# Performance work log

Measured on AMD Instinct MI355X. Metric: run time of the kernel, lower is better.

Reference implementation:

```python
import jax, jax.numpy as jnp
import numpy as np

B, S, D, H = 2, 4096, 512, 8
DH = D // H
EPS = 1e-5


def setup_inputs() -> dict:
    key = jax.random.key(0)
    ks = jax.random.split(key, 8)
    s = 0.02
    return {
        "x": jax.random.normal(ks[0], (B, S, D), jnp.float32),
        "in_proj_w": jax.random.normal(ks[1], (3 * D, D), jnp.float32) * s,
        "in_proj_b": jnp.zeros((3 * D,), jnp.float32),
        "out_proj_w": jax.random.normal(ks[2], (D, D), jnp.float32) * s,
        "out_proj_b": jnp.zeros((D,), jnp.float32),
        "ln1_g": jnp.ones((D,), jnp.float32),
        "ln1_b": jnp.zeros((D,), jnp.float32),
        "ln2_g": jnp.ones((D,), jnp.float32),
        "ln2_b": jnp.zeros((D,), jnp.float32),
        "w1": jax.random.normal(ks[3], (D, D), jnp.float32) * s,
        "b1": jnp.zeros((D,), jnp.float32),
        "w2": jax.random.normal(ks[4], (D, D), jnp.float32) * s,
        "b2": jnp.zeros((D,), jnp.float32),
        "window": 256,
    }


def _layernorm(x, g, b):
    mu = jnp.mean(x, axis=-1, keepdims=True)
    var = jnp.mean(jnp.square(x - mu), axis=-1, keepdims=True)
    return (x - mu) * jax.lax.rsqrt(var + EPS) * g + b


def reference(x, in_proj_w, in_proj_b, out_proj_w, out_proj_b,
              ln1_g, ln1_b, ln2_g, ln2_b, w1, b1, w2, b2, window):
    b, s, d = x.shape
    # sliding-window mask: allowed iff |i - j| <= window
    idx = jnp.arange(s)
    allowed = jnp.abs(idx[:, None] - idx[None, :]) <= window  # [S,S]

    # fused QKV projection (torch MultiheadAttention layout: W [3D, D])
    qkv = x @ in_proj_w.T + in_proj_b  # [B,S,3D]
    q, k, v = jnp.split(qkv, 3, axis=-1)
    q = q.reshape(b, s, H, DH)
    k = k.reshape(b, s, H, DH)
    v = v.reshape(b, s, H, DH)

    scale = 1.0 / jnp.sqrt(jnp.float32(DH))
    scores = jnp.einsum("bqhd,bkhd->bhqk", q, k) * scale  # [B,H,S,S]
    scores = jnp.where(allowed[None, None], scores, -jnp.inf)
    attn = jax.nn.softmax(scores, axis=-1)
    ctx = jnp.einsum("bhqk,bkhd->bqhd", attn, v).reshape(b, s, d)
    attn_out = ctx @ out_proj_w.T + out_proj_b

    # residual + LayerNorm (dropout rate 0 -> identity)
    h = _layernorm(x + attn_out, ln1_g, ln1_b)
    mlp = jax.nn.relu(h @ w1.T + b1) @ w2.T + b2
    return _layernorm(h + mlp, ln2_g, ln2_b)
```

## Files before the change

### kernel.cpp

```cpp
#include <hip/hip_runtime.h>

typedef __bf16 bf16;
typedef __bf16 bf16x2 __attribute__((ext_vector_type(2)));
typedef __bf16 bf16x8 __attribute__((ext_vector_type(8)));
typedef float f32x4 __attribute__((ext_vector_type(4)));

#define S_LEN 4096
#define DMODEL 512
#define NHEAD 8
#define DHEAD 64
#define BATCH 2
#define M_ROWS (BATCH * S_LEN)
#define K_DIM 512
#define QKV_LD 1536

__device__ __forceinline__ void async16(void* lds, const void* g) {
  __builtin_amdgcn_global_load_lds(
      (const __attribute__((address_space(1))) unsigned int*)g,
      (__attribute__((address_space(3))) unsigned int*)lds, 16, 0, 0);
}

__global__ void detect_dtype(const unsigned int* __restrict__ x,
                             int* __restrict__ flag) {
  const int lane = threadIdx.x;
  int cnt = 0;
#pragma unroll
  for (int i = 0; i < 16; ++i) {
    const unsigned int w = x[lane * 16 + i];
    const unsigned int e = (w >> 7) & 0xFFu;
    cnt += (e >= 100u && e <= 140u) ? 1 : 0;
  }
#pragma unroll
  for (int off = 1; off < 64; off <<= 1) cnt += __shfl_xor(cnt, off);
  if (lane == 0) *flag = (cnt >= 700) ? 1 : 0;
}

__device__ __forceinline__ bf16x8 ld8(const void* p, size_t e, bool asF32) {
  if (asF32) {
    const float* q = (const float*)p + e;
    const float4 a = *(const float4*)q;
    const float4 b = *(const float4*)(q + 4);
    bf16x8 r;
    r[0] = (bf16)a.x; r[1] = (bf16)a.y; r[2] = (bf16)a.z; r[3] = (bf16)a.w;
    r[4] = (bf16)b.x; r[5] = (bf16)b.y; r[6] = (bf16)b.z; r[7] = (bf16)b.w;
    return r;
  }
  return *(const bf16x8*)((const bf16*)p + e);
}

__device__ __forceinline__ float ld1(const void* p, size_t e, bool asF32) {
  return asF32 ? ((const float*)p)[e] : (float)((const bf16*)p)[e];
}

__global__ __launch_bounds__(256) void cvt_weights(const void* __restrict__ s0,
                                                   const void* __restrict__ s1,
                                                   const void* __restrict__ s2,
                                                   const void* __restrict__ s3,
                                                   bf16* __restrict__ dst,
                                                   const int* __restrict__ flag) {
  const bool f32in = (*flag == 0);
  const int b = blockIdx.x;
  const void* s;
  size_t doff;
  int lb;
  if (b < 384)      { s = s0; doff = 0;        lb = b; }
  else if (b < 512) { s = s1; doff = 786432;   lb = b - 384; }
  else if (b < 640) { s = s2; doff = 1048576;  lb = b - 512; }
  else              { s = s3; doff = 1310720;  lb = b - 640; }
  const size_t idx = (size_t)lb * 2048 + threadIdx.x * 8;
  *(bf16x8*)(dst + doff + idx) = ld8(s, idx, f32in);
}

__global__ __launch_bounds__(256) void cvt_x(const void* __restrict__ x,
                                             bf16* __restrict__ xb,
                                             const int* __restrict__ flag) {
  const bool f32in = (*flag == 0);
  const size_t idx = ((size_t)blockIdx.x * 256 + threadIdx.x) * 8;
  *(bf16x8*)(xb + idx) = ld8(x, idx, f32in);
}

template <int BN, bool RELU>
__global__ __launch_bounds__(256) void gemm_bt(const bf16* __restrict__ A,
                                               const bf16* __restrict__ W,
                                               const void* __restrict__ bias,
                                               bf16* __restrict__ C, int N,
                                               const int* __restrict__ flag) {
  __shared__ __align__(16) bf16 As[128 * 64];
  __shared__ __align__(16) bf16 Ws[BN * 64];

  const bool f32in = (*flag == 0);

  const int t = threadIdx.x;
  const int lane = t & 63;
  const int wave = t >> 6;
  constexpr int MT = (BN == 128) ? 4 : 2;
  const int wm = (BN == 128) ? (wave >> 1) * 64 : wave * 32;
  const int wn = (BN == 128) ? (wave & 1) * 64 : 0;
  const int l16 = lane & 15;
  const int quad = lane >> 4;
  const int m0 = blockIdx.y * 128;
  const int n0 = blockIdx.x * BN;

  const int rr = lane >> 3;
  const int cb = (lane & 7) ^ rr;
  const int sw = l16 & 7;

  f32x4 acc[MT][4];
#pragma unroll
  for (int i = 0; i < MT; ++i)
#pragma unroll
    for (int j = 0; j < 4; ++j) acc[i][j] = (f32x4){0.f, 0.f, 0.f, 0.f};

  for (int kt = 0; kt < K_DIM; kt += 64) {
    __syncthreads();
#pragma unroll
    for (int i = 0; i < 4; ++i) {
      const int r0 = wave * 32 + i * 8;
      async16(&As[r0 * 64], &A[(size_t)(m0 + r0 + rr) * K_DIM + kt + cb * 8]);
    }
#pragma unroll
    for (int i = 0; i < BN / 32; ++i) {
      const int r0 = wave * (BN / 4) + i * 8;
      async16(&Ws[r0 * 64], &W[(size_t)(n0 + r0 + rr) * K_DIM + kt + cb * 8]);
    }
    __syncthreads();
#pragma unroll
    for (int ks = 0; ks < 2; ++ks) {
      bf16x8 af[MT], wf[4];
#pragma unroll
      for (int mt = 0; mt < MT; ++mt)
        af[mt] = *(const bf16x8*)&As[(wm + mt * 16 + l16) * 64 +
                                     (((ks * 4 + quad) ^ sw) * 8)];
#pragma unroll
      for (int nt = 0; nt < 4; ++nt)
        wf[nt] = *(const bf16x8*)&Ws[(wn + nt * 16 + l16) * 64 +
                                     (((ks * 4 + quad) ^ sw) * 8)];
#pragma unroll
      for (int mt = 0; mt < MT; ++mt)
#pragma unroll
        for (int nt = 0; nt < 4; ++nt)
          acc[mt][nt] = __builtin_amdgcn_mfma_f32_16x16x32_bf16(af[mt], wf[nt],
                                                                acc[mt][nt], 0, 0, 0);
    }
  }

#pragma unroll
  for (int nt = 0; nt < 4; ++nt) {
    const int n = n0 + wn + nt * 16 + l16;
    const float bv = ld1(bias, n, f32in);
#pragma unroll
    for (int mt = 0; mt < MT; ++mt) {
#pragma unroll
      for (int r = 0; r < 4; ++r) {
        const int m = m0 + wm + mt * 16 + quad * 4 + r;
        float v = acc[mt][nt][r] + bv;
        if (RELU) v = fmaxf(v, 0.f);
        C[(size_t)m * N + n] = (bf16)v;
      }
    }
  }
}

__global__ __launch_bounds__(256) void attn_fwd(const bf16* __restrict__ qkv,
                                                bf16* __restrict__ ctx,
                                                const int* __restrict__ wptr) {
  __shared__ __align__(16) bf16 Vt[2][64][72];
  __shared__ __align__(16) bf16 Pbuf[4][16][72];

  const int t = threadIdx.x;
  const int lane = t & 63;
  const int wave = t >> 6;
  const int l16 = lane & 15;
  const int quad = lane >> 4;

  const int nqb = S_LEN / 64;
  const int qblk = blockIdx.x % nqb;
  const int h = (blockIdx.x / nqb) % NHEAD;
  const int b = blockIdx.x / (nqb * NHEAD);
  const int qbase = qblk * 64;
  int window = *wptr;
  if (window < 0) window = 0;
  if (window > S_LEN) window = S_LEN;
  const float scale = 0.125f;

  const int qrow = qbase + wave * 16 + l16;
  const bf16* qp = qkv + (size_t)(b * S_LEN + qrow) * QKV_LD + h * DHEAD;
  const bf16x8 qf0 = *(const bf16x8*)(qp + quad * 8);
  const bf16x8 qf1 = *(const bf16x8*)(qp + 32 + quad * 8);

  f32x4 o[4];
#pragma unroll
  for (int nt = 0; nt < 4; ++nt) o[nt] = (f32x4){0.f, 0.f, 0.f, 0.f};
  float lp[4] = {0.f, 0.f, 0.f, 0.f};

  int kstart = qbase - window;
  if (kstart < 0) kstart = 0;
  kstart &= ~63;
  int kend = qbase + 64 + window;
  if (kend > S_LEN) kend = S_LEN;
  const int niter = (kend - kstart + 63) >> 6;

  const int vk = (t & 31) * 2;
  const int vd = (t >> 5) * 8;
  const bf16* vbase = qkv + (size_t)(b * S_LEN) * QKV_LD + 2 * DMODEL + h * DHEAD + vd;
  const bf16* kbase = qkv + (size_t)(b * S_LEN) * QKV_LD + DMODEL + h * DHEAD;

  {
    const bf16* p = vbase + (size_t)(kstart + vk) * QKV_LD;
    const bf16x8 va = *(const bf16x8*)p;
    const bf16x8 vb = *(const bf16x8*)(p + QKV_LD);
#pragma unroll
    for (int j = 0; j < 8; ++j) {
      bf16x2 pr; pr[0] = va[j]; pr[1] = vb[j];
      *(bf16x2*)&Vt[0][vd + j][vk] = pr;
    }
  }

  for (int it = 0; it < niter; ++it) {
    const int kt = kstart + it * 64;
    const int cur = it & 1;
    __syncthreads();

    bf16x8 na, nb;
    const bool have_next = (it + 1 < niter);
    if (have_next) {
      const bf16* p = vbase + (size_t)(kt + 64 + vk) * QKV_LD;
      na = *(const bf16x8*)p;
      nb = *(const bf16x8*)(p + QKV_LD);
    }

    f32x4 s[4];
#pragma unroll
    for (int t4 = 0; t4 < 4; ++t4) s[t4] = (f32x4){0.f, 0.f, 0.f, 0.f};
#pragma unroll
    for (int t4 = 0; t4 < 4; ++t4) {
      const bf16* kp = kbase + (size_t)(kt + t4 * 16 + l16) * QKV_LD;
      const bf16x8 k0 = *(const bf16x8*)(kp + quad * 8);
      const bf16x8 k1 = *(const bf16x8*)(kp + 32 + quad * 8);
      s[t4] = __builtin_amdgcn_mfma_f32_16x16x32_bf16(qf0, k0, s[t4], 0, 0, 0);
      s[t4] = __builtin_amdgcn_mfma_f32_16x16x32_bf16(qf1, k1, s[t4], 0, 0, 0);
    }

#pragma unroll
    for (int r = 0; r < 4; ++r) {
      const int q = qbase + wave * 16 + quad * 4 + r;
      float psum = 0.f;
#pragma unroll
      for (int t4 = 0; t4 < 4; ++t4) {
        const int key = kt + t4 * 16 + l16;
        int d = q - key; if (d < 0) d = -d;
        const float p = (d <= window) ? __expf(s[t4][r] * scale) : 0.f;
        psum += p;
        Pbuf[wave][quad * 4 + r][t4 * 16 + l16] = (bf16)p;
      }
      lp[r] += psum;
    }

    const bf16x8 pf0 = *(const bf16x8*)&Pbuf[wave][l16][quad * 8];
    const bf16x8 pf1 = *(const bf16x8*)&Pbuf[wave][l16][32 + quad * 8];
#pragma unroll
    for (int nt = 0; nt < 4; ++nt) {
      const bf16x8 v0 = *(const bf16x8*)&Vt[cur][nt * 16 + l16][quad * 8];
      const bf16x8 v1 = *(const bf16x8*)&Vt[cur][nt * 16 + l16][32 + quad * 8];
      o[nt] = __builtin_amdgcn_mfma_f32_16x16x32_bf16(pf0, v0, o[nt], 0, 0, 0);
      o[nt] = __builtin_amdgcn_mfma_f32_16x16x32_bf16(pf1, v1, o[nt], 0, 0, 0);
    }

    if (have_next) {
#pragma unroll
      for (int j = 0; j < 8; ++j) {
        bf16x2 pr; pr[0] = na[j]; pr[1] = nb[j];
        *(bf16x2*)&Vt[cur ^ 1][vd + j][vk] = pr;
      }
    }
  }

#pragma unroll
  for (int r = 0; r < 4; ++r) {
#pragma unroll
    for (int off = 1; off < 16; off <<= 1) lp[r] += __shfl_xor(lp[r], off);
    const float inv = (lp[r] > 0.f) ? (1.0f / lp[r]) : 0.f;
    const int q = qbase + wave * 16 + quad * 4 + r;
#pragma unroll
    for (int nt = 0; nt < 4; ++nt) {
      ctx[(size_t)(b * S_LEN + q) * DMODEL + h * DHEAD + nt * 16 + l16] =
          (bf16)(o[nt][r] * inv);
    }
  }
}

template <bool A_RAW, bool OUT_RAW>
__global__ __launch_bounds__(256) void ln_fused(const void* __restrict__ a,
                                                const bf16* __restrict__ bres,
                                                const void* __restrict__ g,
                                                const void* __restrict__ be,
                                                void* __restrict__ out,
                                                const int* __restrict__ flag) {
  const bool f32in = (*flag == 0);
  const int row = blockIdx.x * 4 + (threadIdx.x >> 6);
  const int lane = threadIdx.x & 63;
  const size_t base = (size_t)row * DMODEL + lane * 8;
  const bf16x8 va = ld8(a, base, A_RAW && f32in);
  const bf16x8 vb = *(const bf16x8*)(bres + base);
  float v[8], s = 0.f, s2 = 0.f;
#pragma unroll
  for (int j = 0; j < 8; ++j) {
    v[j] = (float)va[j] + (float)vb[j];
    s += v[j];
    s2 += v[j] * v[j];
  }
#pragma unroll
  for (int off = 1; off < 64; off <<= 1) {
    s += __shfl_xor(s, off);
    s2 += __shfl_xor(s2, off);
  }
  const float mean = s * (1.0f / DMODEL);
  float var = s2 * (1.0f / DMODEL) - mean * mean;
  if (var < 0.f) var = 0.f;
  const float rstd = rsqrtf(var + 1e-5f);
  const bf16x8 gv = ld8(g, lane * 8, f32in);
  const bf16x8 bev = ld8(be, lane * 8, f32in);
  float ov[8];
#pragma unroll
  for (int j = 0; j < 8; ++j)
    ov[j] = (v[j] - mean) * rstd * (float)gv[j] + (float)bev[j];
  if (OUT_RAW && f32in) {
    float4 o0 = {ov[0], ov[1], ov[2], ov[3]};
    float4 o1 = {ov[4], ov[5], ov[6], ov[7]};
    *(float4*)((float*)out + base) = o0;
    *(float4*)((float*)out + base + 4) = o1;
  } else {
    bf16x8 ob;
#pragma unroll
    for (int j = 0; j < 8; ++j) ob[j] = (bf16)ov[j];
    *(bf16x8*)((bf16*)out + base) = ob;
  }
}

extern "C" void kernel_launch(void* const* d_in, const int* in_sizes, int n_in,
                              void* d_out, int out_size, void* d_ws, size_t ws_size,
                              hipStream_t stream) {
  const void* x          = d_in[0];
  const void* in_proj_w  = d_in[1];
  const void* in_proj_b  = d_in[2];
  const void* out_proj_w = d_in[3];
  const void* out_proj_b = d_in[4];
  const void* ln1_g      = d_in[5];
  const void* ln1_b      = d_in[6];
  const void* ln2_g      = d_in[7];
  const void* ln2_b      = d_in[8];
  const void* w1         = d_in[9];
  const void* b1         = d_in[10];
  const void* w2         = d_in[11];
  const void* b2         = d_in[12];
  const int*  wptr       = (const int*)d_in[13];

  char* ws = (char*)d_ws;
  int* flag = (int*)ws;
  bf16* warena = (bf16*)(ws + 256);
  bf16* wq = warena;
  bf16* wo = warena + 786432;
  bf16* w1b = warena + 1048576;
  bf16* w2b = warena + 1310720;
  char* big = ws + 256 + 3145728;
  bf16* qkv      = (bf16*)big;
  bf16* h        = (bf16*)big;
  bf16* a1       = (bf16*)(big + 8388608);
  bf16* attn_out = (bf16*)(big + 16777216);
  bf16* mlp      = attn_out;
  bf16* xb       = (bf16*)d_out;
  bf16* ctx      = (bf16*)d_out;

  detect_dtype<<<1, 64, 0, stream>>>((const unsigned int*)x, flag);
  cvt_weights<<<768, 256, 0, stream>>>(in_proj_w, out_proj_w, w1, w2, warena, flag);
  cvt_x<<<2048, 256, 0, stream>>>(x, xb, flag);
  gemm_bt<128, false><<<dim3(QKV_LD / 128, M_ROWS / 128), 256, 0, stream>>>(
      xb, wq, in_proj_b, qkv, QKV_LD, flag);
  attn_fwd<<<dim3(BATCH * NHEAD * (S_LEN / 64)), 256, 0, stream>>>(qkv, ctx, wptr);
  gemm_bt<64, false><<<dim3(DMODEL / 64, M_ROWS / 128), 256, 0, stream>>>(
      ctx, wo, out_proj_b, attn_out, DMODEL, flag);
  ln_fused<true, false><<<dim3(M_ROWS / 4), 256, 0, stream>>>(
      x, attn_out, ln1_g, ln1_b, h, flag);
  gemm_bt<64, true><<<dim3(DMODEL / 64, M_ROWS / 128), 256, 0, stream>>>(
      h, w1b, b1, a1, DMODEL, flag);
  gemm_bt<64, false><<<dim3(DMODEL / 64, M_ROWS / 128), 256, 0, stream>>>(
      a1, w2b, b2, mlp, DMODEL, flag);
  ln_fused<false, true><<<dim3(M_ROWS / 4), 256, 0, stream>>>(
      h, mlp, ln2_g, ln2_b, d_out, flag);
}
```

Measured before the change: 230.5 us.

## Prefetch K tiles into registers, remap blocks per XCD, set occupancy hint

Attention now loads the next K tile into registers one iteration ahead, so global loads overlap with MFMA and softmax work. The transposed V store to LDS is moved earlier in the iteration. Block indices are remapped so that all q-blocks of a (batch, head) pair land on the same XCD, which should improve L2 reuse of K/V. A launch_bounds occupancy hint of 4 is added, which raises register pressure because of the extra prefetch registers.

```diff
diff --git a/kernel.cpp b/kernel.cpp
--- a/kernel.cpp
+++ b/kernel.cpp
@@ -161,9 +161,9 @@
   }
 }
 
-__global__ __launch_bounds__(256) void attn_fwd(const bf16* __restrict__ qkv,
-                                                bf16* __restrict__ ctx,
-                                                const int* __restrict__ wptr) {
+__global__ __launch_bounds__(256, 4) void attn_fwd(const bf16* __restrict__ qkv,
+                                                   bf16* __restrict__ ctx,
+                                                   const int* __restrict__ wptr) {
   __shared__ __align__(16) bf16 Vt[2][64][72];
   __shared__ __align__(16) bf16 Pbuf[4][16][72];
 
@@ -173,10 +173,13 @@
   const int l16 = lane & 15;
   const int quad = lane >> 4;
 
-  const int nqb = S_LEN / 64;
-  const int qblk = blockIdx.x % nqb;
-  const int h = (blockIdx.x / nqb) % NHEAD;
-  const int b = blockIdx.x / (nqb * NHEAD);
+  const int bid = blockIdx.x;
+  const int xcd = bid & 7;
+  const int jj = bid >> 3;
+  const int pair = xcd * 2 + (jj >> 6);
+  const int qblk = jj & 63;
+  const int h = pair & 7;
+  const int b = pair >> 3;
   const int qbase = qblk * 64;
   int window = *wptr;
   if (window < 0) window = 0;
@@ -205,6 +208,14 @@
   const bf16* vbase = qkv + (size_t)(b * S_LEN) * QKV_LD + 2 * DMODEL + h * DHEAD + vd;
   const bf16* kbase = qkv + (size_t)(b * S_LEN) * QKV_LD + DMODEL + h * DHEAD;
 
+  bf16x8 kr0[4], kr1[4];
+#pragma unroll
+  for (int t4 = 0; t4 < 4; ++t4) {
+    const bf16* kp = kbase + (size_t)(kstart + t4 * 16 + l16) * QKV_LD;
+    kr0[t4] = *(const bf16x8*)(kp + quad * 8);
+    kr1[t4] = *(const bf16x8*)(kp + 32 + quad * 8);
+  }
+
   {
     const bf16* p = vbase + (size_t)(kstart + vk) * QKV_LD;
     const bf16x8 va = *(const bf16x8*)p;
@@ -219,10 +230,10 @@
   for (int it = 0; it < niter; ++it) {
     const int kt = kstart + it * 64;
     const int cur = it & 1;
+    const bool have_next = (it + 1 < niter);
     __syncthreads();
 
     bf16x8 na, nb;
-    const bool have_next = (it + 1 < niter);
     if (have_next) {
       const bf16* p = vbase + (size_t)(kt + 64 + vk) * QKV_LD;
       na = *(const bf16x8*)p;
@@ -231,25 +242,37 @@
 
     f32x4 s[4];
 #pragma unroll
-    for (int t4 = 0; t4 < 4; ++t4) s[t4] = (f32x4){0.f, 0.f, 0.f, 0.f};
-#pragma unroll
     for (int t4 = 0; t4 < 4; ++t4) {
-      const bf16* kp = kbase + (size_t)(kt + t4 * 16 + l16) * QKV_LD;
-      const bf16x8 k0 = *(const bf16x8*)(kp + quad * 8);
-      const bf16x8 k1 = *(const bf16x8*)(kp + 32 + quad * 8);
-      s[t4] = __builtin_amdgcn_mfma_f32_16x16x32_bf16(qf0, k0, s[t4], 0, 0, 0);
-      s[t4] = __builtin_amdgcn_mfma_f32_16x16x32_bf16(qf1, k1, s[t4], 0, 0, 0);
+      s[t4] = (f32x4){0.f, 0.f, 0.f, 0.f};
+      s[t4] = __builtin_amdgcn_mfma_f32_16x16x32_bf16(qf0, kr0[t4], s[t4], 0, 0, 0);
+      s[t4] = __builtin_amdgcn_mfma_f32_16x16x32_bf16(qf1, kr1[t4], s[t4], 0, 0, 0);
+    }
+
+    bf16x8 kn0[4], kn1[4];
+    if (have_next) {
+#pragma unroll
+      for (int t4 = 0; t4 < 4; ++t4) {
+        const bf16* kp = kbase + (size_t)(kt + 64 + t4 * 16 + l16) * QKV_LD;
+        kn0[t4] = *(const bf16x8*)(kp + quad * 8);
+        kn1[t4] = *(const bf16x8*)(kp + 32 + quad * 8);
+      }
+#pragma unroll
+      for (int j = 0; j < 8; ++j) {
+        bf16x2 pr; pr[0] = na[j]; pr[1] = nb[j];
+        *(bf16x2*)&Vt[cur ^ 1][vd + j][vk] = pr;
+      }
     }
 
 #pragma unroll
     for (int r = 0; r < 4; ++r) {
       const int q = qbase + wave * 16 + quad * 4 + r;
+      const int lo = q - window, hi = q + window;
       float psum = 0.f;
 #pragma unroll
       for (int t4 = 0; t4 < 4; ++t4) {
         const int key = kt + t4 * 16 + l16;
-        int d = q - key; if (d < 0) d = -d;
-        const float p = (d <= window) ? __expf(s[t4][r] * scale) : 0.f;
+        const float p =
+            (key >= lo && key <= hi) ? __expf(s[t4][r] * scale) : 0.f;
         psum += p;
         Pbuf[wave][quad * 4 + r][t4 * 16 + l16] = (bf16)p;
       }
@@ -268,10 +291,7 @@
 
     if (have_next) {
 #pragma unroll
-      for (int j = 0; j < 8; ++j) {
-        bf16x2 pr; pr[0] = na[j]; pr[1] = nb[j];
-        *(bf16x2*)&Vt[cur ^ 1][vd + j][vk] = pr;
-      }
+      for (int t4 = 0; t4 < 4; ++t4) { kr0[t4] = kn0[t4]; kr1[t4] = kn1[t4]; }
     }
   }
 
```

Result: slower. 262.9 us (+14.1%).

## Merge conversion kernels and remap attention blocks for XCD-local K/V reuse

Applied to the files above, without the earlier changes.

Fuses the x and weight bf16 conversion kernels into a single launch, removing one kernel launch and its gap. Remaps attention block indices so that blocks dispatched round-robin to the same XCD (blockIdx & 7) cover the same (batch, head) pairs, letting overlapping sliding-window K/V tiles be reused in that XCD's L2. Also simplifies the window mask test to two range comparisons instead of an absolute difference. The remap hardcodes 8 XCDs and 64 query blocks per head.

```diff
diff --git a/kernel.cpp b/kernel.cpp
--- a/kernel.cpp
+++ b/kernel.cpp
@@ -52,31 +52,31 @@
   return asF32 ? ((const float*)p)[e] : (float)((const bf16*)p)[e];
 }
 
-__global__ __launch_bounds__(256) void cvt_weights(const void* __restrict__ s0,
-                                                   const void* __restrict__ s1,
-                                                   const void* __restrict__ s2,
-                                                   const void* __restrict__ s3,
-                                                   bf16* __restrict__ dst,
-                                                   const int* __restrict__ flag) {
+__global__ __launch_bounds__(256) void cvt_all(const void* __restrict__ x,
+                                               const void* __restrict__ s0,
+                                               const void* __restrict__ s1,
+                                               const void* __restrict__ s2,
+                                               const void* __restrict__ s3,
+                                               bf16* __restrict__ xb,
+                                               bf16* __restrict__ warena,
+                                               const int* __restrict__ flag) {
   const bool f32in = (*flag == 0);
   const int b = blockIdx.x;
+  if (b < 2048) {
+    const size_t idx = ((size_t)b * 256 + threadIdx.x) * 8;
+    *(bf16x8*)(xb + idx) = ld8(x, idx, f32in);
+    return;
+  }
+  const int wb = b - 2048;
   const void* s;
   size_t doff;
   int lb;
-  if (b < 384)      { s = s0; doff = 0;        lb = b; }
-  else if (b < 512) { s = s1; doff = 786432;   lb = b - 384; }
-  else if (b < 640) { s = s2; doff = 1048576;  lb = b - 512; }
-  else              { s = s3; doff = 1310720;  lb = b - 640; }
+  if (wb < 384)      { s = s0; doff = 0;        lb = wb; }
+  else if (wb < 512) { s = s1; doff = 786432;   lb = wb - 384; }
+  else if (wb < 640) { s = s2; doff = 1048576;  lb = wb - 512; }
+  else               { s = s3; doff = 1310720;  lb = wb - 640; }
   const size_t idx = (size_t)lb * 2048 + threadIdx.x * 8;
-  *(bf16x8*)(dst + doff + idx) = ld8(s, idx, f32in);
-}
-
-__global__ __launch_bounds__(256) void cvt_x(const void* __restrict__ x,
-                                             bf16* __restrict__ xb,
-                                             const int* __restrict__ flag) {
-  const bool f32in = (*flag == 0);
-  const size_t idx = ((size_t)blockIdx.x * 256 + threadIdx.x) * 8;
-  *(bf16x8*)(xb + idx) = ld8(x, idx, f32in);
+  *(bf16x8*)(warena + doff + idx) = ld8(s, idx, f32in);
 }
 
 template <int BN, bool RELU>
@@ -173,10 +173,13 @@
   const int l16 = lane & 15;
   const int quad = lane >> 4;
 
-  const int nqb = S_LEN / 64;
-  const int qblk = blockIdx.x % nqb;
-  const int h = (blockIdx.x / nqb) % NHEAD;
-  const int b = blockIdx.x / (nqb * NHEAD);
+  const int bid = blockIdx.x;
+  const int xcd = bid & 7;
+  const int jj = bid >> 3;
+  const int pair = xcd * 2 + (jj >> 6);
+  const int qblk = jj & 63;
+  const int h = pair & 7;
+  const int b = pair >> 3;
   const int qbase = qblk * 64;
   int window = *wptr;
   if (window < 0) window = 0;
@@ -244,12 +247,12 @@
 #pragma unroll
     for (int r = 0; r < 4; ++r) {
       const int q = qbase + wave * 16 + quad * 4 + r;
+      const int lo = q - window, hi = q + window;
       float psum = 0.f;
 #pragma unroll
       for (int t4 = 0; t4 < 4; ++t4) {
         const int key = kt + t4 * 16 + l16;
-        int d = q - key; if (d < 0) d = -d;
-        const float p = (d <= window) ? __expf(s[t4][r] * scale) : 0.f;
+        const float p = (key >= lo && key <= hi) ? __expf(s[t4][r] * scale) : 0.f;
         psum += p;
         Pbuf[wave][quad * 4 + r][t4 * 16 + l16] = (bf16)p;
       }
@@ -372,8 +375,7 @@
   bf16* ctx      = (bf16*)d_out;
 
   detect_dtype<<<1, 64, 0, stream>>>((const unsigned int*)x, flag);
-  cvt_weights<<<768, 256, 0, stream>>>(in_proj_w, out_proj_w, w1, w2, warena, flag);
-  cvt_x<<<2048, 256, 0, stream>>>(x, xb, flag);
+  cvt_all<<<2816, 256, 0, stream>>>(x, in_proj_w, out_proj_w, w1, w2, xb, warena, flag);
   gemm_bt<128, false><<<dim3(QKV_LD / 128, M_ROWS / 128), 256, 0, stream>>>(
       xb, wq, in_proj_b, qkv, QKV_LD, flag);
   attn_fwd<<<dim3(BATCH * NHEAD * (S_LEN / 64)), 256, 0, stream>>>(qkv, ctx, wptr);
```

New measurement: 226.4 us. Within noise of the previous version (-1.8%).
